# Kernel optimization log

Hardware: AMD Instinct MI355X
Metric: run time of the kernel (lower is better)

The kernel has to match this reference:

```python
import jax, jax.numpy as jnp
import numpy as np

B, T, H, V = 16, 128, 512, 32000
BOS = 1

def setup_inputs() -> dict:
    key = jax.random.key(0)
    ks = jax.random.split(key, 18)
    s = 1.0 / np.sqrt(H)
    s2 = 1.0 / np.sqrt(2 * H)
    enc_out = jax.random.normal(ks[0], (B, T, H), dtype=jnp.float32)
    enc_hid = jax.random.normal(ks[1], (1, B, H), dtype=jnp.float32)
    lengths = jax.random.randint(ks[2], (B,), T // 2, T + 1)
    input_mask = (jnp.arange(T)[None, :] < lengths[:, None]).astype(jnp.int32)
    target_tensors = jax.random.randint(ks[3], (B, T), 0, V).astype(jnp.int32)
    return {
        'encoder_outputs': enc_out,
        'encoder_hidden': enc_hid,
        'input_mask': input_mask,
        'target_tensors': target_tensors,
        'emb': jax.random.normal(ks[4], (V, H), dtype=jnp.float32),
        'Wq': jax.random.uniform(ks[5], (H, H), jnp.float32, -s, s),
        'bq': jax.random.uniform(ks[6], (H,), jnp.float32, -s, s),
        'Wv': jax.random.uniform(ks[7], (H, H), jnp.float32, -s, s),
        'bv': jax.random.uniform(ks[8], (H,), jnp.float32, -s, s),
        'Wc': jax.random.uniform(ks[9], (1, H), jnp.float32, -s, s),
        'bc': jax.random.uniform(ks[10], (1,), jnp.float32, -s, s),
        'Wih': jax.random.uniform(ks[11], (3 * H, 2 * H), jnp.float32, -s, s),
        'Whh': jax.random.uniform(ks[12], (3 * H, H), jnp.float32, -s, s),
        'bih': jax.random.uniform(ks[13], (3 * H,), jnp.float32, -s, s),
        'bhh': jax.random.uniform(ks[14], (3 * H,), jnp.float32, -s, s),
        'Wo': jax.random.uniform(ks[15], (V, H), jnp.float32, -s, s),
        'bo': jax.random.uniform(ks[16], (V,), jnp.float32, -s, s),
    }


def reference(encoder_outputs, encoder_hidden, input_mask, target_tensors,
              emb, Wq, bq, Wv, bv, Wc, bc, Wih, Whh, bih, bhh, Wo, bo):
    Bz, Tn, Hn = encoder_outputs.shape
    # values_transformed is invariant across decode steps -> hoist out of loop
    vt = encoder_outputs @ Wv.T + bv  # [B,T,H]
    mask0 = input_mask == 0
    neg = jnp.finfo(encoder_outputs.dtype).min
    # teacher-forced token stream: step t consumes BOS (t=1) then target[:, t-1]
    toks = jnp.concatenate(
        [jnp.full((Bz, 1), BOS, dtype=target_tensors.dtype), target_tensors[:, 1:Tn - 1]], axis=1)  # [B,T-1]
    x_emb = emb[toks]  # [B,T-1,H]
    h0 = encoder_hidden[-1]  # [B,H]

    def step(h, xe):
        # additive (Bahdanau) attention with query = current hidden
        q = h @ Wq.T + bq                                   # [B,H]
        scores = jnp.tanh(q[:, None, :] + vt) @ Wc[0] + bc[0]  # [B,T]
        scores = jnp.where(mask0, neg, scores)
        aw = jax.nn.softmax(scores, axis=1)
        ctx = jnp.einsum('bt,bth->bh', aw, encoder_outputs)  # [B,H]
        x = jnp.concatenate([xe, ctx], axis=-1)              # [B,2H]
        # PyTorch GRU cell
        gi = x @ Wih.T + bih
        gh = h @ Whh.T + bhh
        ir, iz, inn = jnp.split(gi, 3, axis=-1)
        hr, hz, hn = jnp.split(gh, 3, axis=-1)
        r = jax.nn.sigmoid(ir + hr)
        z = jax.nn.sigmoid(iz + hz)
        n = jnp.tanh(inn + r * hn)
        h_new = (1.0 - z) * n + z * h
        logits = h_new @ Wo.T + bo                           # [B,V]
        return h_new, logits

    hT, outs = jax.lax.scan(step, h0, jnp.swapaxes(x_emb, 0, 1))
    outs = jnp.swapaxes(outs, 0, 1)  # [B,T-1,V]
    dec_outputs = jnp.concatenate(
        [jnp.zeros((Bz, 1, outs.shape[-1]), outs.dtype), outs], axis=1)  # [B,T,V]; t=0 stays zero
    return dec_outputs, hT[:, None, :]
```

## Files before the change

kernel.cpp:

```cpp
#include <hip/hip_runtime.h>

typedef unsigned short u16;
typedef unsigned int u32;
typedef short bf16x8 __attribute__((ext_vector_type(8)));
typedef float f32x4 __attribute__((ext_vector_type(4)));

#define B_ 16
#define T_ 128
#define H_ 512
#define V_ 32000
#define G3 1536
#define STEPS 127

#define OFF_VT    0u
#define OFF_P     1048576u
#define OFF_GIX   4194304u
#define OFF_HALL  7340032u
#define OFF_PART  8388608u
#define OFF_BAR   8423424u
#define OFF_AENC  8431616u
#define OFF_AEMB  8955904u
#define OFF_AH    9480192u
#define OFF_BWV   10004480u
#define OFF_BWIH1 10135552u
#define OFF_BWIH2 10528768u
#define OFF_BWO   10921984u

__device__ __forceinline__ u16 f2bf(float f) {
  union { float f; u32 u; } x; x.f = f;
  u32 r = x.u + 0x7fffu + ((x.u >> 16) & 1u);
  return (u16)(r >> 16);
}
__device__ __forceinline__ float bf2f(u16 u) {
  union { u32 u; float f; } x; x.u = ((u32)u) << 16;
  return x.f;
}
__device__ __forceinline__ float wred(float v) {
#pragma unroll
  for (int off = 32; off > 0; off >>= 1) v += __shfl_down(v, off, 64);
  return v;
}

__device__ __forceinline__ void st_sys(float* p, float v) {
  __hip_atomic_store(p, v, __ATOMIC_RELAXED, __HIP_MEMORY_SCOPE_AGENT);
}
__device__ __forceinline__ float ld_sys(const float* p) {
  return __hip_atomic_load(p, __ATOMIC_RELAXED, __HIP_MEMORY_SCOPE_AGENT);
}

__global__ void k_init(float* __restrict__ out, u32* __restrict__ bars) {
  int idx = blockIdx.x * 256 + threadIdx.x;
  if (idx < 512000) {
    int b = idx / 32000; int v = idx - b * 32000;
    out[(size_t)b * 4096000 + v] = 0.f;
  }
  if (idx < 512) bars[idx] = 0u;
}

__global__ void k_f2bf(const float* __restrict__ src, u16* __restrict__ dst, int n) {
  int idx = blockIdx.x * 256 + threadIdx.x;
  if (idx < n) dst[idx] = f2bf(src[idx]);
}

__global__ void k_f2bf_sub(const float* __restrict__ src, u16* __restrict__ dst,
                           int n, int ld, int off) {
  int idx = blockIdx.x * 256 + threadIdx.x;
  if (idx < n) {
    int r = idx >> 9, c = idx & 511;
    dst[idx] = f2bf(src[(size_t)r * ld + off + c]);
  }
}

__global__ void k_gather(const float* __restrict__ emb, const int* __restrict__ tgt,
                         u16* __restrict__ dst, int n) {
  int idx = blockIdx.x * 256 + threadIdx.x;
  if (idx < n) {
    int m = idx >> 9, c = idx & 511;
    int b = m & 15, s = m >> 4;
    int tok = (s == 0) ? 1 : tgt[b * 128 + s];
    dst[idx] = f2bf(emb[(size_t)tok * 512 + c]);
  }
}

__global__ __launch_bounds__(256) void gemm_bf16(
    const u16* __restrict__ A, const u16* __restrict__ Bm,
    const float* __restrict__ bias, float* __restrict__ C,
    int ldc, int mode) {
  __shared__ u16 As[128 * 32];
  __shared__ u16 Bs[128 * 32];
  const int tid = threadIdx.x;
  const int lane = tid & 63;
  const int wave = tid >> 6;
  const int lr = lane & 15;
  const int quad = lane >> 4;
  const int wm = (wave >> 1) * 64;
  const int wn = (wave & 1) * 64;
  const int bm = blockIdx.y * 128;
  const int bn = blockIdx.x * 128;
  const int srow = tid >> 1;
  const int shalf = (tid & 1) * 16;

  f32x4 acc[4][4];
#pragma unroll
  for (int i = 0; i < 4; ++i)
#pragma unroll
    for (int j = 0; j < 4; ++j) acc[i][j] = (f32x4){0.f, 0.f, 0.f, 0.f};

  for (int kt = 0; kt < 16; ++kt) {
    const u16* gA = A + (size_t)(bm + srow) * 512 + kt * 32 + shalf;
    const u16* gB = Bm + (size_t)(bn + srow) * 512 + kt * 32 + shalf;
    uint4 a0 = *(const uint4*)gA;
    uint4 a1 = *(const uint4*)(gA + 8);
    uint4 b0 = *(const uint4*)gB;
    uint4 b1 = *(const uint4*)(gB + 8);
    __syncthreads();
    *(uint4*)&As[srow * 32 + shalf] = a0;
    *(uint4*)&As[srow * 32 + shalf + 8] = a1;
    *(uint4*)&Bs[srow * 32 + shalf] = b0;
    *(uint4*)&Bs[srow * 32 + shalf + 8] = b1;
    __syncthreads();
    bf16x8 af[4], bf[4];
#pragma unroll
    for (int i = 0; i < 4; ++i)
      af[i] = *(const bf16x8*)&As[(wm + i * 16 + lr) * 32 + quad * 8];
#pragma unroll
    for (int j = 0; j < 4; ++j)
      bf[j] = *(const bf16x8*)&Bs[(wn + j * 16 + lr) * 32 + quad * 8];
#pragma unroll
    for (int i = 0; i < 4; ++i)
#pragma unroll
      for (int j = 0; j < 4; ++j)
        acc[i][j] = __builtin_amdgcn_mfma_f32_16x16x32_bf16(af[i], bf[j], acc[i][j], 0, 0, 0);
  }

#pragma unroll
  for (int j = 0; j < 4; ++j) {
    int ng = bn + wn + j * 16 + lr;
    float bv = bias ? bias[ng] : 0.f;
#pragma unroll
    for (int i = 0; i < 4; ++i) {
      int mg0 = bm + wm + i * 16 + quad * 4;
#pragma unroll
      for (int r = 0; r < 4; ++r) {
        int mg = mg0 + r;
        float v = acc[i][j][r] + bv;
        if (mode == 0) {
          C[(size_t)mg * ldc + ng] = v;
        } else {
          if (mg < 2032) {
            int s = mg >> 4, b = mg & 15;
            C[(size_t)((b << 7) + s + 1) * 32000 + ng] = v;
          }
        }
      }
    }
  }
}

__device__ __forceinline__ void gbar_g(u32* gb, int j, u32 phase) {
  __syncthreads();
  if (threadIdx.x == 0) {
    asm volatile("s_waitcnt vmcnt(0)" ::: "memory");
    __hip_atomic_store(&gb[j], phase, __ATOMIC_RELAXED, __HIP_MEMORY_SCOPE_AGENT);
  }
  if (threadIdx.x < 64) {
    for (;;) {
      u32 v = __hip_atomic_load(&gb[threadIdx.x & 15], __ATOMIC_RELAXED, __HIP_MEMORY_SCOPE_AGENT);
      if (__all(v >= phase)) break;
      __builtin_amdgcn_s_sleep(1);
    }
  }
  asm volatile("" ::: "memory");
  __syncthreads();
}

__global__ __launch_bounds__(256, 1) void seq_kernel(
    const float* __restrict__ Wq, const float* __restrict__ bq,
    const float* __restrict__ Wc, const float* __restrict__ bc,
    const float* __restrict__ Whh, const float* __restrict__ bhh,
    const float* __restrict__ h0, const int* __restrict__ mask,
    const float* __restrict__ ws_vt, const float* __restrict__ ws_P,
    const float* __restrict__ ws_gix, float* __restrict__ ws_hall,
    float* __restrict__ ws_part, u32* __restrict__ bars,
    float* __restrict__ outT) {
  const int k = blockIdx.x;
  const int b = k >> 4;
  const int j = k & 15;
  const int i0 = j << 5;
  const int tid = threadIdx.x;
  const int lane = tid & 63;
  const int wv = tid >> 6;

  __shared__ u16 P_lds[128][96];
  __shared__ float vt_s[32][128];
  __shared__ float h_l[512];
  __shared__ float q_l[32];
  __shared__ float gh_l[96];
  __shared__ float gi_l[96];
  __shared__ float s_lds[128];
  __shared__ float p_lds[128];
  __shared__ float Wc_s[32];
  __shared__ float bq_s[32];
  __shared__ float bhh_s[96];
  __shared__ int   m_l[128];

  float Wreg[32][8];
#pragma unroll
  for (int rr = 0; rr < 32; ++rr) {
    const float* wp = (wv == 0) ? (Wq + (size_t)(i0 + rr) * 512)
                                : (Whh + (size_t)((wv - 1) * 512 + i0 + rr) * 512);
    const float4* w4 = (const float4*)(wp + (lane << 3));
    float4 a = w4[0], c = w4[1];
    Wreg[rr][0] = a.x; Wreg[rr][1] = a.y; Wreg[rr][2] = a.z; Wreg[rr][3] = a.w;
    Wreg[rr][4] = c.x; Wreg[rr][5] = c.y; Wreg[rr][6] = c.z; Wreg[rr][7] = c.w;
  }
  if (tid < 32) { Wc_s[tid] = Wc[i0 + tid]; bq_s[tid] = bq[i0 + tid]; }
  if (tid < 96) bhh_s[tid] = bhh[(tid >> 5) * 512 + i0 + (tid & 31)];
  if (tid < 128) m_l[tid] = mask[(b << 7) + tid];
  for (int idx = tid; idx < 128 * 96; idx += 256) {
    int t = idx / 96; int jj = idx - t * 96;
    int col = (jj >> 5) * 512 + i0 + (jj & 31);
    P_lds[t][jj] = f2bf(ws_P[(size_t)((b << 7) + t) * 1536 + col]);
  }
  for (int idx = tid; idx < 32 * 128; idx += 256) {
    int rr = idx >> 7, t = idx & 127;
    vt_s[rr][t] = ws_vt[(size_t)((b << 7) + t) * 512 + i0 + rr];
  }
  const float bc0 = bc[0];
  __syncthreads();

  u32* gb = bars + (b << 5);
  u32 phase = 0;
  for (int s = 0; s < STEPS; ++s) {
    const float* hbase = (s == 0) ? (h0 + (b << 9))
                                  : (ws_hall + (size_t)(((s - 1) << 4) + b) * 512);
    for (int i = tid; i < 512; i += 256) h_l[i] = ld_sys(hbase + i);
    __syncthreads();
    float hk[8];
    {
      const float4* h4 = (const float4*)&h_l[lane << 3];
      float4 a = h4[0], c = h4[1];
      hk[0] = a.x; hk[1] = a.y; hk[2] = a.z; hk[3] = a.w;
      hk[4] = c.x; hk[5] = c.y; hk[6] = c.z; hk[7] = c.w;
    }
#pragma unroll
    for (int rr = 0; rr < 32; ++rr) {
      float p = Wreg[rr][0] * hk[0] + Wreg[rr][1] * hk[1]
              + Wreg[rr][2] * hk[2] + Wreg[rr][3] * hk[3]
              + Wreg[rr][4] * hk[4] + Wreg[rr][5] * hk[5]
              + Wreg[rr][6] * hk[6] + Wreg[rr][7] * hk[7];
      p = wred(p);
      if (lane == 0) {
        if (wv == 0) q_l[rr] = p;
        else gh_l[((wv - 1) << 5) + rr] = p + bhh_s[((wv - 1) << 5) + rr];
      }
    }
    __syncthreads();
    {
      int t = tid >> 1, rh = (tid & 1) << 4;
      float part = 0.f;
#pragma unroll
      for (int u = 0; u < 16; ++u) {
        int rr = rh + u;
        part += Wc_s[rr] * tanhf(q_l[rr] + bq_s[rr] + vt_s[rr][t]);
      }
      part += __shfl_xor(part, 1, 64);
      if (!(tid & 1)) st_sys(&ws_part[(size_t)(((b << 4) + j) << 7) + t], part);
    }
    gbar_g(gb, j, ++phase);

    {
      int t = tid >> 1;
      int ib = (tid & 1) << 3;
      float sum = 0.f;
#pragma unroll
      for (int u = 0; u < 8; ++u)
        sum += ld_sys(&ws_part[(size_t)(((b << 4) + ib + u) << 7) + t]);
      sum += __shfl_xor(sum, 1, 64);
      if (!(tid & 1))
        s_lds[t] = m_l[t] ? (sum + bc0) : -3.4028234663852886e+38f;
    }
    __syncthreads();
    float vm = fmaxf(s_lds[lane], s_lds[64 + lane]);
#pragma unroll
    for (int mo = 32; mo > 0; mo >>= 1) vm = fmaxf(vm, __shfl_xor(vm, mo, 64));
    if (tid < 128) p_lds[tid] = expf(s_lds[tid] - vm);
    __syncthreads();
    float vs = p_lds[lane] + p_lds[64 + lane];
#pragma unroll
    for (int mo = 32; mo > 0; mo >>= 1) vs += __shfl_xor(vs, mo, 64);
    float rsum = 1.0f / vs;
    if (tid < 96) {
      int jg = (tid >> 5) * 512 + i0 + (tid & 31);
      float acc = 0.f;
#pragma unroll 8
      for (int t = 0; t < 128; ++t) acc += p_lds[t] * bf2f(P_lds[t][tid]);
      gi_l[tid] = ws_gix[(size_t)((s << 4) + b) * 1536 + jg] + acc * rsum;
    }
    __syncthreads();
    if (tid < 32) {
      float rg = 1.f / (1.f + expf(-(gi_l[tid] + gh_l[tid])));
      float zg = 1.f / (1.f + expf(-(gi_l[32 + tid] + gh_l[32 + tid])));
      float ng = tanhf(gi_l[64 + tid] + rg * gh_l[64 + tid]);
      float hold = h_l[i0 + tid];
      float hn = (1.f - zg) * ng + zg * hold;
      st_sys(&ws_hall[(size_t)((s << 4) + b) * 512 + i0 + tid], hn);
    }
    gbar_g(gb, j, ++phase);
  }

  if (j == 0) {
    for (int i = tid; i < 512; i += 256)
      outT[(b << 9) + i] = ld_sys(&ws_hall[(size_t)(126 * 16 + b) * 512 + i]);
  }
}

extern "C" void kernel_launch(void* const* d_in, const int* in_sizes, int n_in,
                              void* d_out, int out_size, void* d_ws, size_t ws_size,
                              hipStream_t stream) {
  const float* enc  = (const float*)d_in[0];
  const float* ehid = (const float*)d_in[1];
  const int*   mask = (const int*)d_in[2];
  const int*   tgt  = (const int*)d_in[3];
  const float* emb  = (const float*)d_in[4];
  const float* Wq   = (const float*)d_in[5];
  const float* bq   = (const float*)d_in[6];
  const float* Wv   = (const float*)d_in[7];
  const float* bv   = (const float*)d_in[8];
  const float* Wc   = (const float*)d_in[9];
  const float* bc   = (const float*)d_in[10];
  const float* Wih  = (const float*)d_in[11];
  const float* Whh  = (const float*)d_in[12];
  const float* bih  = (const float*)d_in[13];
  const float* bhh  = (const float*)d_in[14];
  const float* Wo   = (const float*)d_in[15];
  const float* bo   = (const float*)d_in[16];

  float* out = (float*)d_out;
  float* ws  = (float*)d_ws;
  float* vt   = ws + OFF_VT;
  float* P    = ws + OFF_P;
  float* gix  = ws + OFF_GIX;
  float* hall = ws + OFF_HALL;
  float* part = ws + OFF_PART;
  u32*   bars = (u32*)(ws + OFF_BAR);
  u16* A_enc = (u16*)(ws + OFF_AENC);
  u16* A_emb = (u16*)(ws + OFF_AEMB);
  u16* A_h   = (u16*)(ws + OFF_AH);
  u16* B_wv  = (u16*)(ws + OFF_BWV);
  u16* B_wi1 = (u16*)(ws + OFF_BWIH1);
  u16* B_wi2 = (u16*)(ws + OFF_BWIH2);
  u16* B_wo  = (u16*)(ws + OFF_BWO);

  k_init<<<2000, 256, 0, stream>>>(out, bars);
  k_f2bf<<<4096, 256, 0, stream>>>(enc, A_enc, 1048576);
  k_f2bf<<<1024, 256, 0, stream>>>(Wv, B_wv, 262144);
  k_f2bf_sub<<<3072, 256, 0, stream>>>(Wih, B_wi1, 786432, 1024, 0);
  k_f2bf_sub<<<3072, 256, 0, stream>>>(Wih, B_wi2, 786432, 1024, 512);
  k_f2bf<<<64000, 256, 0, stream>>>(Wo, B_wo, 16384000);
  k_gather<<<4064, 256, 0, stream>>>(emb, tgt, A_emb, 1040384);

  gemm_bf16<<<dim3(4, 16), 256, 0, stream>>>(A_enc, B_wv, bv, vt, 512, 0);
  gemm_bf16<<<dim3(12, 16), 256, 0, stream>>>(A_enc, B_wi2, nullptr, P, 1536, 0);
  gemm_bf16<<<dim3(12, 16), 256, 0, stream>>>(A_emb, B_wi1, bih, gix, 1536, 0);

  seq_kernel<<<256, 256, 0, stream>>>(Wq, bq, Wc, bc, Whh, bhh,
                                      ehid, mask, vt, P, gix, hall, part, bars,
                                      out + 65536000);

  k_f2bf<<<4064, 256, 0, stream>>>(hall, A_h, 1040384);
  gemm_bf16<<<dim3(250, 16), 256, 0, stream>>>(A_h, B_wo, bo, out, 32000, 1);
}
```

Baseline: 3.282 ms.

## Move Whh GEMV off critical path into LDS bf16, overlap with barrier, fast math

The Wq projection is spread across all four waves before the attention scores, so the first step finishes sooner. The Whh·h product is stored as bf16 in LDS and computed after the score partials are published, which lets it overlap the wait at the cross-block barrier. tanh, sigmoid and exp switch to fast __expf-based approximations. The costs are bf16 rounding of Whh, lower transcendental accuracy, and about 96KB of extra LDS.

```diff
diff --git a/kernel.cpp b/kernel.cpp
--- a/kernel.cpp
+++ b/kernel.cpp
@@ -39,6 +39,14 @@
 #pragma unroll
   for (int off = 32; off > 0; off >>= 1) v += __shfl_down(v, off, 64);
   return v;
+}
+__device__ __forceinline__ float tanh_fast(float x) {
+  float cx = fminf(8.f, fmaxf(-8.f, x));
+  float e = __expf(2.f * cx);
+  return (e - 1.f) / (e + 1.f);
+}
+__device__ __forceinline__ float sigmoid_fast(float x) {
+  return 1.f / (1.f + __expf(-x));
 }
 
 __device__ __forceinline__ void st_sys(float* p, float v) {
@@ -191,6 +199,7 @@
   const int lane = tid & 63;
   const int wv = tid >> 6;
 
+  __shared__ u16 Whh_s[96 * 512];
   __shared__ u16 P_lds[128][96];
   __shared__ float vt_s[32][128];
   __shared__ float h_l[512];
@@ -204,19 +213,23 @@
   __shared__ float bhh_s[96];
   __shared__ int   m_l[128];
 
-  float Wreg[32][8];
-#pragma unroll
-  for (int rr = 0; rr < 32; ++rr) {
-    const float* wp = (wv == 0) ? (Wq + (size_t)(i0 + rr) * 512)
-                                : (Whh + (size_t)((wv - 1) * 512 + i0 + rr) * 512);
+  float Wq_reg[8][8];
+#pragma unroll
+  for (int rr = 0; rr < 8; ++rr) {
+    const float* wp = Wq + (size_t)(i0 + (wv << 3) + rr) * 512;
     const float4* w4 = (const float4*)(wp + (lane << 3));
     float4 a = w4[0], c = w4[1];
-    Wreg[rr][0] = a.x; Wreg[rr][1] = a.y; Wreg[rr][2] = a.z; Wreg[rr][3] = a.w;
-    Wreg[rr][4] = c.x; Wreg[rr][5] = c.y; Wreg[rr][6] = c.z; Wreg[rr][7] = c.w;
+    Wq_reg[rr][0] = a.x; Wq_reg[rr][1] = a.y; Wq_reg[rr][2] = a.z; Wq_reg[rr][3] = a.w;
+    Wq_reg[rr][4] = c.x; Wq_reg[rr][5] = c.y; Wq_reg[rr][6] = c.z; Wq_reg[rr][7] = c.w;
   }
   if (tid < 32) { Wc_s[tid] = Wc[i0 + tid]; bq_s[tid] = bq[i0 + tid]; }
   if (tid < 96) bhh_s[tid] = bhh[(tid >> 5) * 512 + i0 + (tid & 31)];
   if (tid < 128) m_l[tid] = mask[(b << 7) + tid];
+  for (int idx = tid; idx < 96 * 512; idx += 256) {
+    int rw = idx >> 9, col = idx & 511;
+    int grow = ((rw >> 5) << 9) + i0 + (rw & 31);
+    Whh_s[idx] = f2bf(Whh[(size_t)grow * 512 + col]);
+  }
   for (int idx = tid; idx < 128 * 96; idx += 256) {
     int t = idx / 96; int jj = idx - t * 96;
     int col = (jj >> 5) * 512 + i0 + (jj & 31);
@@ -234,7 +247,8 @@
   for (int s = 0; s < STEPS; ++s) {
     const float* hbase = (s == 0) ? (h0 + (b << 9))
                                   : (ws_hall + (size_t)(((s - 1) << 4) + b) * 512);
-    for (int i = tid; i < 512; i += 256) h_l[i] = ld_sys(hbase + i);
+    h_l[tid] = ld_sys(hbase + tid);
+    h_l[tid + 256] = ld_sys(hbase + tid + 256);
     __syncthreads();
     float hk[8];
     {
@@ -244,15 +258,15 @@
       hk[4] = c.x; hk[5] = c.y; hk[6] = c.z; hk[7] = c.w;
     }
 #pragma unroll
-    for (int rr = 0; rr < 32; ++rr) {
-      float p = Wreg[rr][0] * hk[0] + Wreg[rr][1] * hk[1]
-              + Wreg[rr][2] * hk[2] + Wreg[rr][3] * hk[3]
-              + Wreg[rr][4] * hk[4] + Wreg[rr][5] * hk[5]
-              + Wreg[rr][6] * hk[6] + Wreg[rr][7] * hk[7];
+    for (int rr = 0; rr < 8; ++rr) {
+      float p = Wq_reg[rr][0] * hk[0] + Wq_reg[rr][1] * hk[1]
+              + Wq_reg[rr][2] * hk[2] + Wq_reg[rr][3] * hk[3]
+              + Wq_reg[rr][4] * hk[4] + Wq_reg[rr][5] * hk[5]
+              + Wq_reg[rr][6] * hk[6] + Wq_reg[rr][7] * hk[7];
       p = wred(p);
       if (lane == 0) {
-        if (wv == 0) q_l[rr] = p;
-        else gh_l[((wv - 1) << 5) + rr] = p + bhh_s[((wv - 1) << 5) + rr];
+        int rq = (wv << 3) + rr;
+        q_l[rq] = p + bq_s[rq];
       }
     }
     __syncthreads();
@@ -262,10 +276,26 @@
 #pragma unroll
       for (int u = 0; u < 16; ++u) {
         int rr = rh + u;
-        part += Wc_s[rr] * tanhf(q_l[rr] + bq_s[rr] + vt_s[rr][t]);
+        part += Wc_s[rr] * tanh_fast(q_l[rr] + vt_s[rr][t]);
       }
       part += __shfl_xor(part, 1, 64);
       if (!(tid & 1)) st_sys(&ws_part[(size_t)(((b << 4) + j) << 7) + t], part);
+    }
+#pragma unroll 4
+    for (int rr = 0; rr < 24; ++rr) {
+      int rw = wv * 24 + rr;
+      bf16x8 w = *(const bf16x8*)&Whh_s[rw * 512 + (lane << 3)];
+      const u32* wu = (const u32*)&w;
+      float p = 0.f;
+#pragma unroll
+      for (int e = 0; e < 4; ++e) {
+        u32 g = wu[e];
+        union { u32 u; float f; } lo, hi;
+        lo.u = g << 16; hi.u = g & 0xffff0000u;
+        p += lo.f * hk[2 * e] + hi.f * hk[2 * e + 1];
+      }
+      p = wred(p);
+      if (lane == 0) gh_l[rw] = p + bhh_s[rw];
     }
     gbar_g(gb, j, ++phase);
 
@@ -284,7 +314,7 @@
     float vm = fmaxf(s_lds[lane], s_lds[64 + lane]);
 #pragma unroll
     for (int mo = 32; mo > 0; mo >>= 1) vm = fmaxf(vm, __shfl_xor(vm, mo, 64));
-    if (tid < 128) p_lds[tid] = expf(s_lds[tid] - vm);
+    if (tid < 128) p_lds[tid] = __expf(s_lds[tid] - vm);
     __syncthreads();
     float vs = p_lds[lane] + p_lds[64 + lane];
 #pragma unroll
@@ -299,9 +329,9 @@
     }
     __syncthreads();
     if (tid < 32) {
-      float rg = 1.f / (1.f + expf(-(gi_l[tid] + gh_l[tid])));
-      float zg = 1.f / (1.f + expf(-(gi_l[32 + tid] + gh_l[32 + tid])));
-      float ng = tanhf(gi_l[64 + tid] + rg * gh_l[64 + tid]);
+      float rg = sigmoid_fast(gi_l[tid] + gh_l[tid]);
+      float zg = sigmoid_fast(gi_l[32 + tid] + gh_l[32 + tid]);
+      float ng = tanh_fast(gi_l[64 + tid] + rg * gh_l[64 + tid]);
       float hold = h_l[i0 + tid];
       float hn = (1.f - zg) * ng + zg * hold;
       st_sys(&ws_hall[(size_t)((s << 4) + b) * 512 + i0 + tid], hn);
```

New measurement: 2.733 ms. 16.7% less time.
